# Optimization experiments

Hardware: AMD Instinct MI355X
Metric: run time of the kernel (lower is better)

Reference implementation:

```python
import jax, jax.numpy as jnp
import numpy as np

N_NODES = 100000
N_EDGES = 3200000
IN_FEAT = 128
HIDDEN = 128
CLASSES = 32


def gcn_conv(x, edge_index, W, b, n_nodes):
    """PyG GCNConv: linear -> symmetric-normalized scatter-add with self-loops -> +bias."""
    src, dst = edge_index[0], edge_index[1]
    loop = jnp.arange(n_nodes, dtype=edge_index.dtype)
    src = jnp.concatenate([src, loop])
    dst = jnp.concatenate([dst, loop])
    # degree (with self-loops) on destination nodes
    deg = jax.ops.segment_sum(jnp.ones_like(dst, dtype=x.dtype), dst, num_segments=n_nodes)
    dinv = jnp.where(deg > 0, jax.lax.rsqrt(deg), 0.0)
    norm = dinv[src] * dinv[dst]  # [E+N]
    h = x @ W  # [N, out]
    msg = h[src] * norm[:, None]  # gather + scale, [E+N, out]
    out = jax.ops.segment_sum(msg, dst, num_segments=n_nodes)  # scatter-add
    return out + b


def setup_inputs() -> dict:
    key = jax.random.key(0)
    k1, k2, k3, k4 = jax.random.split(key, 4)
    x = jax.random.normal(k1, (N_NODES, IN_FEAT), dtype=jnp.float32)
    edge_index = jax.random.randint(k2, (2, N_EDGES), 0, N_NODES, dtype=jnp.int64)
    W1 = jax.random.normal(k3, (IN_FEAT, HIDDEN), dtype=jnp.float32) / np.sqrt(IN_FEAT)
    b1 = jnp.zeros((HIDDEN,), dtype=jnp.float32)
    W2 = jax.random.normal(k4, (HIDDEN, CLASSES), dtype=jnp.float32) / np.sqrt(HIDDEN)
    b2 = jnp.zeros((CLASSES,), dtype=jnp.float32)
    return {"x": x, "edge_index": edge_index, "W1": W1, "b1": b1, "W2": W2, "b2": b2}


def reference(x, edge_index, W1, b1, W2, b2):
    n = x.shape[0]
    h = gcn_conv(x, edge_index, W1, b1, n)
    h = jax.nn.relu(h)
    # dropout p=0.5 is identity in eval mode
    out = gcn_conv(h, edge_index, W2, b2, n)
    return out
```

## Files before the change

### kernel.cpp

```cpp
#include <hip/hip_runtime.h>

#define N_NODES 100000
#define N_EDGES 3200000
#define F_IN 128
#define F_HID 128
#define F_OUT 32
#define CAP 96

#define NBUCK 1563
#define CAPB 2432
#define EPT 32

#define BM 128
#define BK 16

typedef float f32x2 __attribute__((ext_vector_type(2)));

__device__ inline unsigned pack_bf16(float a, float b) {
    unsigned ua = __float_as_uint(a);
    ua = (ua + 0x7fffu + ((ua >> 16) & 1u)) >> 16;
    unsigned ub = __float_as_uint(b);
    ub = (ub + 0x7fffu + ((ub >> 16) & 1u)) >> 16;
    return ua | (ub << 16);
}
__device__ inline float lo16(unsigned u) { return __uint_as_float(u << 16); }
__device__ inline float hi16(unsigned u) { return __uint_as_float(u & 0xffff0000u); }

__global__ __launch_bounds__(256) void k_part(const int* __restrict__ ei,
                                              int* __restrict__ gcur,
                                              unsigned* __restrict__ stage) {
    __shared__ int cnt[NBUCK];
    __shared__ int base[NBUCK];
    int tid = threadIdx.x;
    for (int i = tid; i < NBUCK; i += 256) cnt[i] = 0;
    __syncthreads();

    long e0 = (long)blockIdx.x * (256 * EPT);
    int dcache[EPT];
#pragma unroll
    for (int i = 0; i < EPT; ++i) {
        long e = e0 + i * 256 + tid;
        int d = (e < N_EDGES) ? ei[N_EDGES + e] : -1;
        dcache[i] = d;
        if (d >= 0) atomicAdd(&cnt[d >> 6], 1);
    }
    __syncthreads();
    for (int i = tid; i < NBUCK; i += 256) {
        base[i] = atomicAdd(&gcur[i], cnt[i]);
        cnt[i] = 0;
    }
    __syncthreads();
#pragma unroll
    for (int i = 0; i < EPT; ++i) {
        long e = e0 + i * 256 + tid;
        int d = dcache[i];
        if (d >= 0) {
            int s = ei[e];
            int b = d >> 6;
            int pos = base[b] + atomicAdd(&cnt[b], 1);
            if (pos < CAPB)
                stage[(size_t)b * CAPB + pos] = ((unsigned)(d & 63) << 17) | (unsigned)s;
        }
    }
}

__global__ __launch_bounds__(256) void k_csr(const unsigned* __restrict__ stage,
                                             const int* __restrict__ gcur,
                                             int* __restrict__ csr,
                                             int* __restrict__ deg,
                                             float* __restrict__ dinv) {
    __shared__ int cnt[64];
    int b = blockIdx.x;
    int tid = threadIdx.x;
    if (tid < 64) cnt[tid] = 0;
    __syncthreads();

    int d0 = b << 6;
    int m = gcur[b];
    if (m > CAPB) m = CAPB;
    const unsigned* sp = stage + (size_t)b * CAPB;
    for (int i = tid; i < m; i += 256) {
        unsigned rec = __builtin_nontemporal_load(sp + i);
        int s = (int)(rec & 0x1ffffu);
        int dl = (int)(rec >> 17);
        int pos = atomicAdd(&cnt[dl], 1);
        if (pos < CAP) csr[(size_t)(d0 + dl) * CAP + pos] = s;
    }
    __syncthreads();
    if (tid < 64) {
        int dd = d0 + tid;
        if (dd < N_NODES) {
            int dg = cnt[tid];
            deg[dd] = dg;
            dinv[dd] = rsqrtf((float)(dg + 1));
        }
    }
}

__global__ __launch_bounds__(256) void k_gemm1(const float* __restrict__ x,
                                               const float* __restrict__ W1,
                                               const float* __restrict__ dinv,
                                               unsigned* __restrict__ g1u) {
    __shared__ float xT[BK][BM + 8];
    __shared__ float wt[BK][F_HID];

    int tid = threadIdx.x;
    int m0 = blockIdx.x * BM;

    int rg = tid >> 4;
    int cg = tid & 15;
    int r0 = rg * 8;
    int c0 = cg * 8;

    int lr = tid >> 1;
    int lk = (tid & 1) * 8;
    int gr = m0 + lr;
    int grc = gr < N_NODES ? gr : N_NODES - 1;
    const float* xrow = x + (size_t)grc * F_IN + lk;

    float acc[8][8];
#pragma unroll
    for (int i = 0; i < 8; ++i)
#pragma unroll
        for (int j = 0; j < 8; ++j) acc[i][j] = 0.f;

    for (int k0 = 0; k0 < F_IN; k0 += BK) {
        float4 v0 = *(const float4*)(xrow + k0);
        float4 v1 = *(const float4*)(xrow + k0 + 4);
        const float4* w4 = (const float4*)(W1 + (size_t)k0 * F_HID);
        float4 wv0 = w4[tid];
        float4 wv1 = w4[tid + 256];

        xT[lk + 0][lr] = v0.x; xT[lk + 1][lr] = v0.y;
        xT[lk + 2][lr] = v0.z; xT[lk + 3][lr] = v0.w;
        xT[lk + 4][lr] = v1.x; xT[lk + 5][lr] = v1.y;
        xT[lk + 6][lr] = v1.z; xT[lk + 7][lr] = v1.w;
        ((float4*)wt)[tid] = wv0;
        ((float4*)wt)[tid + 256] = wv1;
        __syncthreads();

#pragma unroll
        for (int k = 0; k < BK; ++k) {
            float a[8], b[8];
            *(float4*)(a + 0) = *(const float4*)&xT[k][r0];
            *(float4*)(a + 4) = *(const float4*)&xT[k][r0 + 4];
            *(float4*)(b + 0) = *(const float4*)&wt[k][c0];
            *(float4*)(b + 4) = *(const float4*)&wt[k][c0 + 4];
#pragma unroll
            for (int i = 0; i < 8; ++i)
#pragma unroll
                for (int j = 0; j < 8; ++j)
                    acc[i][j] = fmaf(a[i], b[j], acc[i][j]);
        }
        __syncthreads();
    }

#pragma unroll
    for (int i = 0; i < 8; ++i) {
        int n = m0 + r0 + i;
        if (n < N_NODES) {
            float s = dinv[n];
            uint4 o;
            o.x = pack_bf16(acc[i][0] * s, acc[i][1] * s);
            o.y = pack_bf16(acc[i][2] * s, acc[i][3] * s);
            o.z = pack_bf16(acc[i][4] * s, acc[i][5] * s);
            o.w = pack_bf16(acc[i][6] * s, acc[i][7] * s);
            *(uint4*)(g1u + (size_t)n * 64 + (c0 >> 1)) = o;
        }
    }
}

__global__ __launch_bounds__(256) void k_pull1_gemm2(const int* __restrict__ csr,
                                                     const int* __restrict__ deg_i,
                                                     const unsigned* __restrict__ g1u,
                                                     const float* __restrict__ dinv,
                                                     const float* __restrict__ b1,
                                                     const float* __restrict__ W2,
                                                     unsigned* __restrict__ g2u) {
    __shared__ float w2l[F_HID * F_OUT];
    __shared__ unsigned alu[16][64];
    {
        const float4* w4 = (const float4*)W2;
        float4* wl4 = (float4*)w2l;
#pragma unroll
        for (int i = 0; i < 4; ++i)
            wl4[threadIdx.x + i * 256] = w4[threadIdx.x + i * 256];
    }
    int lane = threadIdx.x & 63;
    int wv = threadIdx.x >> 6;
    int nb4 = __builtin_amdgcn_readfirstlane(blockIdx.x * 16 + wv * 4);

    int4 deg4 = *(const int4*)(deg_i + nb4);
    float4 di4 = *(const float4*)(dinv + nb4);
    float2 bb = *(const float2*)(b1 + lane * 2);

#define GATHER(S, ACC)                                            \
    {                                                             \
        const unsigned* p = g1u + ((size_t)(unsigned)(S) << 6);   \
        unsigned v = p[lane];                                     \
        ACC += (f32x2){lo16(v), hi16(v)};                         \
    }

#pragma unroll
    for (int i = 0; i < 4; ++i) {
        int n = nb4 + i;
        int deg = ((const int*)&deg4)[i];
        if (deg > CAP) deg = CAP;
        const int* crow = csr + (size_t)n * CAP;
        int sidx0 = (lane < deg) ? __builtin_nontemporal_load(crow + lane) : 0;

        unsigned us = g1u[(size_t)n * 64 + lane];
        f32x2 ac0 = (f32x2){lo16(us), hi16(us)};
        f32x2 ac1 = (f32x2){0.f, 0.f}, ac2 = ac1, ac3 = ac1;

        int m1 = deg < 64 ? deg : 64;
        int j = 0;
        for (; j + 3 < m1; j += 4) {
            int s0 = __builtin_amdgcn_readlane(sidx0, j);
            int s1 = __builtin_amdgcn_readlane(sidx0, j + 1);
            int s2 = __builtin_amdgcn_readlane(sidx0, j + 2);
            int s3 = __builtin_amdgcn_readlane(sidx0, j + 3);
            GATHER(s0, ac0) GATHER(s1, ac1) GATHER(s2, ac2) GATHER(s3, ac3)
        }
        for (; j < m1; ++j) {
            int s0 = __builtin_amdgcn_readlane(sidx0, j);
            GATHER(s0, ac0)
        }
        if (deg > 64) {
            int sidx1 = __builtin_nontemporal_load(crow + 64 + (lane & 31));
            int m2 = deg - 64;
            for (j = 0; j < m2; ++j) {
                int s0 = __builtin_amdgcn_readlane(sidx1, j);
                GATHER(s0, ac0)
            }
        }
        f32x2 a = (ac0 + ac1) + (ac2 + ac3);
        float di = ((const float*)&di4)[i];
        float a0 = fmaxf(fmaf(di, a.x, bb.x), 0.f);
        float a1 = fmaxf(fmaf(di, a.y, bb.y), 0.f);
        alu[wv * 4 + i][lane] = pack_bf16(a0, a1);
    }
#undef GATHER
    __syncthreads();

    int jj = lane & 31, kh = lane >> 5;
    f32x2 s0 = {0.f, 0.f}, s1 = s0, s2 = s0, s3 = s0;
#pragma unroll 4
    for (int k2 = 0; k2 < 32; ++k2) {
        int k = kh * 64 + k2 * 2;
        f32x2 w = (f32x2){w2l[k * F_OUT + jj], w2l[(k + 1) * F_OUT + jj]};
        int ki = kh * 32 + k2;
        unsigned p0 = alu[wv * 4 + 0][ki];
        unsigned p1 = alu[wv * 4 + 1][ki];
        unsigned p2 = alu[wv * 4 + 2][ki];
        unsigned p3 = alu[wv * 4 + 3][ki];
        s0 += (f32x2){lo16(p0), hi16(p0)} * w;
        s1 += (f32x2){lo16(p1), hi16(p1)} * w;
        s2 += (f32x2){lo16(p2), hi16(p2)} * w;
        s3 += (f32x2){lo16(p3), hi16(p3)} * w;
    }
    float r0 = s0.x + s0.y, r1 = s1.x + s1.y, r2 = s2.x + s2.y, r3 = s3.x + s3.y;
    r0 += __shfl_xor(r0, 32); r1 += __shfl_xor(r1, 32);
    r2 += __shfl_xor(r2, 32); r3 += __shfl_xor(r3, 32);
    r0 *= ((const float*)&di4)[0]; r1 *= ((const float*)&di4)[1];
    r2 *= ((const float*)&di4)[2]; r3 *= ((const float*)&di4)[3];

    int fl16 = lane & 15;
    float sa0 = __shfl(r0, fl16 * 2), sb0 = __shfl(r0, fl16 * 2 + 1);
    float sa1 = __shfl(r1, fl16 * 2), sb1 = __shfl(r1, fl16 * 2 + 1);
    float sa2 = __shfl(r2, fl16 * 2), sb2 = __shfl(r2, fl16 * 2 + 1);
    float sa3 = __shfl(r3, fl16 * 2), sb3 = __shfl(r3, fl16 * 2 + 1);
    if (lane < 16) {
        g2u[(size_t)(nb4 + 0) * 16 + fl16] = pack_bf16(sa0, sb0);
        g2u[(size_t)(nb4 + 1) * 16 + fl16] = pack_bf16(sa1, sb1);
        g2u[(size_t)(nb4 + 2) * 16 + fl16] = pack_bf16(sa2, sb2);
        g2u[(size_t)(nb4 + 3) * 16 + fl16] = pack_bf16(sa3, sb3);
    }
}

__global__ __launch_bounds__(256) void k_pull2(const int* __restrict__ csr,
                                               const int* __restrict__ deg_i,
                                               const unsigned* __restrict__ g2u,
                                               const float* __restrict__ dinv,
                                               const float* __restrict__ b2,
                                               float* __restrict__ out) {
    int lane = threadIdx.x & 63;
    int wv = threadIdx.x >> 6;
    int qw = lane >> 4, fl = lane & 15;
    int n = blockIdx.x * 16 + wv * 4 + qw;

    unsigned u0 = g2u[(size_t)n * 16 + fl];
    float a0x = lo16(u0), a0y = hi16(u0);
    float a1x = 0.f, a1y = 0.f, a2x = 0.f, a2y = 0.f, a3x = 0.f, a3y = 0.f;
    int deg = deg_i[n];
    if (deg > CAP) deg = CAP;
    const int* crow = csr + (size_t)n * CAP;
    for (int e0 = 0; e0 < deg; e0 += 16) {
        int rem = deg - e0;
        int m = rem < 16 ? rem : 16;
        int sidx = (fl < m) ? __builtin_nontemporal_load(crow + e0 + fl) : 0;
        int j = 0;
        for (; j + 3 < m; j += 4) {
            int s0 = __shfl(sidx, j, 16);
            int s1 = __shfl(sidx, j + 1, 16);
            int s2 = __shfl(sidx, j + 2, 16);
            int s3 = __shfl(sidx, j + 3, 16);
            unsigned v0 = g2u[(unsigned)s0 * 16u + fl];
            unsigned v1 = g2u[(unsigned)s1 * 16u + fl];
            unsigned v2 = g2u[(unsigned)s2 * 16u + fl];
            unsigned v3 = g2u[(unsigned)s3 * 16u + fl];
            a0x += lo16(v0); a0y += hi16(v0);
            a1x += lo16(v1); a1y += hi16(v1);
            a2x += lo16(v2); a2y += hi16(v2);
            a3x += lo16(v3); a3y += hi16(v3);
        }
        for (; j < m; ++j) {
            int s0 = __shfl(sidx, j, 16);
            unsigned v0 = g2u[(unsigned)s0 * 16u + fl];
            a0x += lo16(v0); a0y += hi16(v0);
        }
    }
    float ax = (a0x + a1x) + (a2x + a3x);
    float ay = (a0y + a1y) + (a2y + a3y);

    float di = dinv[n];
    float2 bb = *(const float2*)(b2 + fl * 2);
    f32x2 o;
    o.x = fmaf(di, ax, bb.x);
    o.y = fmaf(di, ay, bb.y);
    __builtin_nontemporal_store(o, (f32x2*)(out + (size_t)n * F_OUT + fl * 2));
}

extern "C" void kernel_launch(void* const* d_in, const int* in_sizes, int n_in,
                              void* d_out, int out_size, void* d_ws, size_t ws_size,
                              hipStream_t stream) {
    const float* x  = (const float*)d_in[0];
    const int*   ei = (const int*)d_in[1];
    const float* W1 = (const float*)d_in[2];
    const float* b1 = (const float*)d_in[3];
    const float* W2 = (const float*)d_in[4];
    const float* b2 = (const float*)d_in[5];
    float* out = (float*)d_out;

    char* ws = (char*)d_ws;
    int*      deg   = (int*)(ws);
    float*    dinv  = (float*)(ws + 524288);
    int*      gcur  = (int*)(ws + 1048576);
    int*      csr   = (int*)(ws + 1572864);
    unsigned* stage = (unsigned*)(ws + 40000000);
    unsigned* g1u   = (unsigned*)(ws + 55204864);
    unsigned* g2u   = (unsigned*)(ws + 80804864);

    (void)hipMemsetAsync(gcur, 0, NBUCK * sizeof(int), stream);
    k_part<<<(N_EDGES + 256 * EPT - 1) / (256 * EPT), 256, 0, stream>>>(ei, gcur, stage);
    k_csr<<<NBUCK, 256, 0, stream>>>(stage, gcur, csr, deg, dinv);

    k_gemm1<<<(N_NODES + BM - 1) / BM, 256, 0, stream>>>(x, W1, dinv, g1u);

    k_pull1_gemm2<<<N_NODES / 16, 256, 0, stream>>>(csr, deg, g1u, dinv, b1, W2, g2u);
    k_pull2<<<N_NODES / 16, 256, 0, stream>>>(csr, deg, g2u, dinv, b2, out);
}
```

Before: 297.1 us.

## Fuse CSR build with first GEMM and vectorize edge partition loads

The per-bucket CSR kernel now also computes the first linear layer for its 64 nodes. It uses the freshly computed dinv from shared memory to scale and pack the bf16 output, so one launch and a dinv round trip disappear. The edge partition kernel now reads destination and source indices with int4 loads over 4096-edge blocks instead of scalar loads over 8192-edge blocks, which doubles the grid size. The GEMM tile shrinks from 128 to 64 rows, which lowers W1 reuse per block. The partition kernel only handles whole 1024-edge chunks, so any leftover tail is dropped; that is harmless only because the edge count divides evenly.

Measured after the change: 301.4 us. About the same (+1.5%).

```diff
diff --git a/kernel.cpp b/kernel.cpp
--- a/kernel.cpp
+++ b/kernel.cpp
@@ -9,9 +9,7 @@
 
 #define NBUCK 1563
 #define CAPB 2432
-#define EPT 32
-
-#define BM 128
+
 #define BK 16
 
 typedef float f32x2 __attribute__((ext_vector_type(2)));
@@ -35,41 +33,59 @@
     for (int i = tid; i < NBUCK; i += 256) cnt[i] = 0;
     __syncthreads();
 
-    long e0 = (long)blockIdx.x * (256 * EPT);
-    int dcache[EPT];
-#pragma unroll
-    for (int i = 0; i < EPT; ++i) {
-        long e = e0 + i * 256 + tid;
-        int d = (e < N_EDGES) ? ei[N_EDGES + e] : -1;
-        dcache[i] = d;
-        if (d >= 0) atomicAdd(&cnt[d >> 6], 1);
-    }
+    long e0 = (long)blockIdx.x * 4096;
+    long rem = N_EDGES - e0;
+    const int4* d4 = (const int4*)(ei + N_EDGES + e0);
+    const int4* s4 = (const int4*)(ei + e0);
+    int4 dc0, dc1, dc2, dc3;
+
+#define HIST(DC, I)                                                     \
+    if ((I + 1) * 1024 <= rem) {                                        \
+        DC = d4[I * 256 + tid];                                         \
+        atomicAdd(&cnt[DC.x >> 6], 1); atomicAdd(&cnt[DC.y >> 6], 1);   \
+        atomicAdd(&cnt[DC.z >> 6], 1); atomicAdd(&cnt[DC.w >> 6], 1);   \
+    }
+    HIST(dc0, 0) HIST(dc1, 1) HIST(dc2, 2) HIST(dc3, 3)
+#undef HIST
     __syncthreads();
     for (int i = tid; i < NBUCK; i += 256) {
         base[i] = atomicAdd(&gcur[i], cnt[i]);
         cnt[i] = 0;
     }
     __syncthreads();
-#pragma unroll
-    for (int i = 0; i < EPT; ++i) {
-        long e = e0 + i * 256 + tid;
-        int d = dcache[i];
-        if (d >= 0) {
-            int s = ei[e];
-            int b = d >> 6;
-            int pos = base[b] + atomicAdd(&cnt[b], 1);
-            if (pos < CAPB)
-                stage[(size_t)b * CAPB + pos] = ((unsigned)(d & 63) << 17) | (unsigned)s;
-        }
-    }
-}
-
-__global__ __launch_bounds__(256) void k_csr(const unsigned* __restrict__ stage,
-                                             const int* __restrict__ gcur,
-                                             int* __restrict__ csr,
-                                             int* __restrict__ deg,
-                                             float* __restrict__ dinv) {
+
+#define PLACE(D, S)                                                     \
+    {                                                                   \
+        int b_ = (D) >> 6;                                              \
+        int pos_ = base[b_] + atomicAdd(&cnt[b_], 1);                   \
+        if (pos_ < CAPB)                                                \
+            stage[(size_t)b_ * CAPB + pos_] =                           \
+                ((unsigned)((D) & 63) << 17) | (unsigned)(S);           \
+    }
+#define WR(DC, I)                                                       \
+    if ((I + 1) * 1024 <= rem) {                                        \
+        int4 sv = s4[I * 256 + tid];                                    \
+        PLACE(DC.x, sv.x) PLACE(DC.y, sv.y)                             \
+        PLACE(DC.z, sv.z) PLACE(DC.w, sv.w)                             \
+    }
+    WR(dc0, 0) WR(dc1, 1) WR(dc2, 2) WR(dc3, 3)
+#undef WR
+#undef PLACE
+}
+
+__global__ __launch_bounds__(256) void k_csr_gemm1(const unsigned* __restrict__ stage,
+                                                   const int* __restrict__ gcur,
+                                                   int* __restrict__ csr,
+                                                   int* __restrict__ deg,
+                                                   float* __restrict__ dinv,
+                                                   const float* __restrict__ x,
+                                                   const float* __restrict__ W1,
+                                                   unsigned* __restrict__ g1u) {
     __shared__ int cnt[64];
+    __shared__ float dv[64];
+    __shared__ float xT[BK][68];
+    __shared__ float wt[BK][F_HID];
+
     int b = blockIdx.x;
     int tid = threadIdx.x;
     if (tid < 64) cnt[tid] = 0;
@@ -89,77 +105,67 @@
     __syncthreads();
     if (tid < 64) {
         int dd = d0 + tid;
+        float di = 0.f;
         if (dd < N_NODES) {
             int dg = cnt[tid];
             deg[dd] = dg;
-            dinv[dd] = rsqrtf((float)(dg + 1));
-        }
-    }
-}
-
-__global__ __launch_bounds__(256) void k_gemm1(const float* __restrict__ x,
-                                               const float* __restrict__ W1,
-                                               const float* __restrict__ dinv,
-                                               unsigned* __restrict__ g1u) {
-    __shared__ float xT[BK][BM + 8];
-    __shared__ float wt[BK][F_HID];
-
-    int tid = threadIdx.x;
-    int m0 = blockIdx.x * BM;
+            di = rsqrtf((float)(dg + 1));
+            dinv[dd] = di;
+        }
+        dv[tid] = di;
+    }
 
     int rg = tid >> 4;
     int cg = tid & 15;
-    int r0 = rg * 8;
+    int r0 = rg * 4;
     int c0 = cg * 8;
 
-    int lr = tid >> 1;
-    int lk = (tid & 1) * 8;
-    int gr = m0 + lr;
+    int lr = tid >> 2;
+    int lk = (tid & 3) * 4;
+    int gr = d0 + lr;
     int grc = gr < N_NODES ? gr : N_NODES - 1;
     const float* xrow = x + (size_t)grc * F_IN + lk;
 
-    float acc[8][8];
-#pragma unroll
-    for (int i = 0; i < 8; ++i)
+    float acc[4][8];
+#pragma unroll
+    for (int i = 0; i < 4; ++i)
 #pragma unroll
         for (int j = 0; j < 8; ++j) acc[i][j] = 0.f;
 
     for (int k0 = 0; k0 < F_IN; k0 += BK) {
-        float4 v0 = *(const float4*)(xrow + k0);
-        float4 v1 = *(const float4*)(xrow + k0 + 4);
+        float4 v = *(const float4*)(xrow + k0);
         const float4* w4 = (const float4*)(W1 + (size_t)k0 * F_HID);
         float4 wv0 = w4[tid];
         float4 wv1 = w4[tid + 256];
 
-        xT[lk + 0][lr] = v0.x; xT[lk + 1][lr] = v0.y;
-        xT[lk + 2][lr] = v0.z; xT[lk + 3][lr] = v0.w;
-        xT[lk + 4][lr] = v1.x; xT[lk + 5][lr] = v1.y;
-        xT[lk + 6][lr] = v1.z; xT[lk + 7][lr] = v1.w;
+        xT[lk + 0][lr] = v.x;
+        xT[lk + 1][lr] = v.y;
+        xT[lk + 2][lr] = v.z;
+        xT[lk + 3][lr] = v.w;
         ((float4*)wt)[tid] = wv0;
         ((float4*)wt)[tid + 256] = wv1;
         __syncthreads();
 
 #pragma unroll
         for (int k = 0; k < BK; ++k) {
-            float a[8], b[8];
-            *(float4*)(a + 0) = *(const float4*)&xT[k][r0];
-            *(float4*)(a + 4) = *(const float4*)&xT[k][r0 + 4];
-            *(float4*)(b + 0) = *(const float4*)&wt[k][c0];
-            *(float4*)(b + 4) = *(const float4*)&wt[k][c0 + 4];
-#pragma unroll
-            for (int i = 0; i < 8; ++i)
+            float a[4], bb[8];
+            *(float4*)a = *(const float4*)&xT[k][r0];
+            *(float4*)(bb + 0) = *(const float4*)&wt[k][c0];
+            *(float4*)(bb + 4) = *(const float4*)&wt[k][c0 + 4];
+#pragma unroll
+            for (int i = 0; i < 4; ++i)
 #pragma unroll
                 for (int j = 0; j < 8; ++j)
-                    acc[i][j] = fmaf(a[i], b[j], acc[i][j]);
+                    acc[i][j] = fmaf(a[i], bb[j], acc[i][j]);
         }
         __syncthreads();
     }
 
 #pragma unroll
-    for (int i = 0; i < 8; ++i) {
-        int n = m0 + r0 + i;
+    for (int i = 0; i < 4; ++i) {
+        int n = d0 + r0 + i;
         if (n < N_NODES) {
-            float s = dinv[n];
+            float s = dv[r0 + i];
             uint4 o;
             o.x = pack_bf16(acc[i][0] * s, acc[i][1] * s);
             o.y = pack_bf16(acc[i][2] * s, acc[i][3] * s);
@@ -352,10 +358,8 @@
     unsigned* g2u   = (unsigned*)(ws + 80804864);
 
     (void)hipMemsetAsync(gcur, 0, NBUCK * sizeof(int), stream);
-    k_part<<<(N_EDGES + 256 * EPT - 1) / (256 * EPT), 256, 0, stream>>>(ei, gcur, stage);
-    k_csr<<<NBUCK, 256, 0, stream>>>(stage, gcur, csr, deg, dinv);
-
-    k_gemm1<<<(N_NODES + BM - 1) / BM, 256, 0, stream>>>(x, W1, dinv, g1u);
+    k_part<<<(N_EDGES + 4095) / 4096, 256, 0, stream>>>(ei, gcur, stage);
+    k_csr_gemm1<<<NBUCK, 256, 0, stream>>>(stage, gcur, csr, deg, dinv, x, W1, g1u);
 
     k_pull1_gemm2<<<N_NODES / 16, 256, 0, stream>>>(csr, deg, g1u, dinv, b1, W2, g2u);
     k_pull2<<<N_NODES / 16, 256, 0, stream>>>(csr, deg, g2u, dinv, b2, out);
```
